# Kernel tuning notes

Hardware: AMD Instinct MI355X
Metric: run time of the kernel (lower is better)

## Reference

```python
import jax, jax.numpy as jnp
import numpy as np

UNITS = 512
BACKCAST_LEN = 512
FORECAST_LEN = 128
NB_HARMONICS = 64  # forecast_length // 2
THETAS_DIM = 2 * NB_HARMONICS
BATCH = 16384


def _seasonality_basis(length, nb_harmonics):
    # t = 2*pi*arange(L)/L ; rows interleaved [cos(0*t), sin(0*t), cos(1*t), sin(1*t), ...]
    t = 2.0 * np.pi * jnp.arange(length, dtype=jnp.float32) / length
    i = jnp.arange(nb_harmonics, dtype=jnp.float32)[:, None]  # [H,1]
    angles = i * t[None, :]                                   # [H,L]
    basis = jnp.stack([jnp.cos(angles), jnp.sin(angles)], axis=1)  # [H,2,L]
    return basis.reshape(2 * nb_harmonics, length)            # [2H,L]


def setup_inputs() -> dict:
    key = jax.random.key(0)
    ks = jax.random.split(key, 10)
    s_in = 1.0 / np.sqrt(BACKCAST_LEN)
    s_u = 1.0 / np.sqrt(UNITS)
    return {
        "x": jax.random.normal(ks[0], (BATCH, BACKCAST_LEN), jnp.float32),
        "W1": jax.random.normal(ks[1], (UNITS, BACKCAST_LEN), jnp.float32) * s_in,
        "b1": jax.random.normal(ks[2], (UNITS,), jnp.float32) * s_in,
        "W2": jax.random.normal(ks[3], (UNITS, UNITS), jnp.float32) * s_u,
        "b2": jax.random.normal(ks[4], (UNITS,), jnp.float32) * s_u,
        "W3": jax.random.normal(ks[5], (UNITS, UNITS), jnp.float32) * s_u,
        "b3": jax.random.normal(ks[6], (UNITS,), jnp.float32) * s_u,
        "W4": jax.random.normal(ks[7], (UNITS, UNITS), jnp.float32) * s_u,
        "b4": jax.random.normal(ks[8], (UNITS,), jnp.float32) * s_u,
        "Wt": jax.random.normal(ks[9], (THETAS_DIM, UNITS), jnp.float32) * s_u,
    }


def reference(x, W1, b1, W2, b2, W3, b3, W4, b4, Wt):
    h = jax.nn.relu(x @ W1.T + b1)
    h = jax.nn.relu(h @ W2.T + b2)
    h = jax.nn.relu(h @ W3.T + b3)
    h = jax.nn.relu(h @ W4.T + b4)
    theta = h @ Wt.T  # [B, 2H], shared thetas (share_thetas=True)
    basis_b = _seasonality_basis(BACKCAST_LEN, NB_HARMONICS)  # [2H, Lb]
    basis_f = _seasonality_basis(FORECAST_LEN, NB_HARMONICS)  # [2H, Lf]
    backcast = theta @ basis_b  # [B, Lb]
    forecast = theta @ basis_f  # [B, Lf]
    return (backcast, forecast)
```

## Files before the change

kernel.cpp:

```cpp
#include <hip/hip_runtime.h>
#include <hip/hip_bf16.h>
#include <math.h>


#define BATCH 16384
#define ROWS  64

typedef __bf16 bf16x8 __attribute__((ext_vector_type(8)));
typedef float  f32x4  __attribute__((ext_vector_type(4)));

__device__ __forceinline__ unsigned short f2bf(float f) {
  union { float f; unsigned u; } v; v.f = f;
  unsigned r = v.u + 0x7fff + ((v.u >> 16) & 1);
  return (unsigned short)(r >> 16);
}

__global__ __launch_bounds__(256) void prep_kernel(
    const float* __restrict__ W1, const float* __restrict__ W2,
    const float* __restrict__ W3, const float* __restrict__ W4,
    const float* __restrict__ Wt,
    unsigned short* __restrict__ W1p, unsigned short* __restrict__ W2p,
    unsigned short* __restrict__ W3p, unsigned short* __restrict__ W4p,
    unsigned short* __restrict__ Wtp,
    unsigned short* __restrict__ basp) {
  const int t = blockIdx.x * 256 + threadIdx.x;
  if (t < 139264) {
    const float* src; unsigned short* dst; int u;
    if (t < 131072) {
      const int w = t >> 15; u = t & 32767;
      src = (w == 0) ? W1 : (w == 1) ? W2 : (w == 2) ? W3 : W4;
      dst = (w == 0) ? W1p : (w == 1) ? W2p : (w == 2) ? W3p : W4p;
    } else {
      u = t - 131072; src = Wt; dst = Wtp;
    }
    const int lane = u & 63, ks = (u >> 6) & 15, cf = u >> 10;
    const int col = cf * 16 + (lane & 15);
    const int k0  = ks * 32 + (lane >> 4) * 8;
    const float4* s = (const float4*)(src + (size_t)col * 512 + k0);
    const float4 a = s[0], b = s[1];
    uint4 o;
    o.x = f2bf(a.x) | ((unsigned)f2bf(a.y) << 16);
    o.y = f2bf(a.z) | ((unsigned)f2bf(a.w) << 16);
    o.z = f2bf(b.x) | ((unsigned)f2bf(b.y) << 16);
    o.w = f2bf(b.z) | ((unsigned)f2bf(b.w) << 16);
    ((uint4*)dst)[u] = o;
  } else if (t < 149504) {
    const int u = t - 139264;
    const int lane = u & 63, ks = (u >> 6) & 3, cf = u >> 8;
    const int col = cf * 16 + (lane & 15);
    const int r0  = ks * 32 + (lane >> 4) * 8;
    int l, L;
    if (col < 512) { l = col; L = 512; } else { l = col - 512; L = 128; }
    const float w0 = 6.283185307179586f * (float)l / (float)L;
    unsigned short e[8];
#pragma unroll
    for (int i = 0; i < 8; ++i) {
      const int r = r0 + i;
      const float ang = (float)(r >> 1) * w0;
      e[i] = f2bf((r & 1) ? sinf(ang) : cosf(ang));
    }
    uint4 o;
    o.x = e[0] | ((unsigned)e[1] << 16);
    o.y = e[2] | ((unsigned)e[3] << 16);
    o.z = e[4] | ((unsigned)e[5] << 16);
    o.w = e[6] | ((unsigned)e[7] << 16);
    ((uint4*)basp)[u] = o;
  }
}

__device__ __forceinline__ void layer512(
    unsigned short* hA, const bf16x8* __restrict__ Wp,
    const float* __restrict__ bias, const int wv, const int lane) {
  const int l15 = lane & 15, g = lane >> 4;
  int rb[4], am[4];
#pragma unroll
  for (int m = 0; m < 4; ++m) {
    const int row = m * 16 + l15;
    rb[m] = row * 1024;
    am[m] = (row & 7) << 4;
  }
  f32x4 acc[4][4];
#pragma unroll
  for (int m = 0; m < 4; ++m)
#pragma unroll
    for (int n = 0; n < 4; ++n) acc[m][n] = (f32x4){0.f, 0.f, 0.f, 0.f};

  const bf16x8* base = Wp + (size_t)wv * 4096 + lane;

  bf16x8 bv[4][4];
#pragma unroll
  for (int s = 0; s < 3; ++s)
#pragma unroll
    for (int n = 0; n < 4; ++n) bv[s][n] = base[n * 1024 + s * 64];

#pragma unroll
  for (int ks = 0; ks < 16; ++ks) {
    if (ks < 13) {
#pragma unroll
      for (int n = 0; n < 4; ++n)
        bv[(ks + 3) & 3][n] = base[n * 1024 + (ks + 3) * 64];
    }
    bf16x8 av[4];
    const int kb = ks * 64 + g * 16;
#pragma unroll
    for (int m = 0; m < 4; ++m)
      av[m] = *(const bf16x8*)((const char*)hA + rb[m] + (kb ^ am[m]));
    __builtin_amdgcn_s_setprio(1);
#pragma unroll
    for (int m = 0; m < 4; ++m)
#pragma unroll
      for (int n = 0; n < 4; ++n)
        acc[m][n] = __builtin_amdgcn_mfma_f32_16x16x32_bf16(av[m], bv[ks & 3][n], acc[m][n], 0, 0, 0);
    __builtin_amdgcn_s_setprio(0);
  }

  __syncthreads();
#pragma unroll
  for (int n = 0; n < 4; ++n) {
    const int col = wv * 64 + n * 16 + l15;
    const float bvv = bias[col];
#pragma unroll
    for (int m = 0; m < 4; ++m)
#pragma unroll
      for (int r = 0; r < 4; ++r) {
        const int row = m * 16 + g * 4 + r;
        const float v = fmaxf(acc[m][n][r] + bvv, 0.f);
        *(unsigned short*)((char*)hA + row * 1024 + ((col * 2) ^ ((row & 7) << 4))) = f2bf(v);
      }
  }
  __syncthreads();
}

__global__ __launch_bounds__(512, 2) void fused_nbeats(
    const float* __restrict__ x,
    const bf16x8* __restrict__ W1p, const float* __restrict__ b1,
    const bf16x8* __restrict__ W2p, const float* __restrict__ b2,
    const bf16x8* __restrict__ W3p, const float* __restrict__ b3,
    const bf16x8* __restrict__ W4p, const float* __restrict__ b4,
    const bf16x8* __restrict__ Wtp,
    const bf16x8* __restrict__ basp,
    float* __restrict__ out) {
  __shared__ __align__(16) unsigned short hA[ROWS * 512];

  const int tid  = threadIdx.x;
  const int lane = tid & 63;
  const int wv   = tid >> 6;
  const int l15  = lane & 15, g = lane >> 4;
  const int r0   = blockIdx.x * ROWS;

  {
    const float4* xs = (const float4*)(x + (size_t)r0 * 512);
#pragma unroll
    for (int j = 0; j < 16; ++j) {
      const int f = tid + j * 512;
      const int row = f >> 7, c4 = f & 127;
      const float4 v = xs[f];
      uint2 o;
      o.x = f2bf(v.x) | ((unsigned)f2bf(v.y) << 16);
      o.y = f2bf(v.z) | ((unsigned)f2bf(v.w) << 16);
      *(uint2*)((char*)hA + row * 1024 + ((c4 * 8) ^ ((row & 7) << 4))) = o;
    }
  }
  __syncthreads();

  layer512(hA, W1p, b1, wv, lane);
  layer512(hA, W2p, b2, wv, lane);
  layer512(hA, W3p, b3, wv, lane);
  layer512(hA, W4p, b4, wv, lane);

  {
    int rb[4], am[4];
#pragma unroll
    for (int m = 0; m < 4; ++m) {
      const int row = m * 16 + l15;
      rb[m] = row * 1024;
      am[m] = (row & 7) << 4;
    }
    f32x4 tacc[4];
#pragma unroll
    for (int m = 0; m < 4; ++m) tacc[m] = (f32x4){0.f, 0.f, 0.f, 0.f};
    const bf16x8* tb = Wtp + (size_t)wv * 1024 + lane;
    bf16x8 tv[4];
#pragma unroll
    for (int s = 0; s < 3; ++s) tv[s] = tb[s * 64];
#pragma unroll
    for (int ks = 0; ks < 16; ++ks) {
      if (ks < 13) tv[(ks + 3) & 3] = tb[(ks + 3) * 64];
      bf16x8 av[4];
      const int kb = ks * 64 + g * 16;
#pragma unroll
      for (int m = 0; m < 4; ++m)
        av[m] = *(const bf16x8*)((const char*)hA + rb[m] + (kb ^ am[m]));
      __builtin_amdgcn_s_setprio(1);
#pragma unroll
      for (int m = 0; m < 4; ++m)
        tacc[m] = __builtin_amdgcn_mfma_f32_16x16x32_bf16(av[m], tv[ks & 3], tacc[m], 0, 0, 0);
      __builtin_amdgcn_s_setprio(0);
    }
    __syncthreads();
#pragma unroll
    for (int m = 0; m < 4; ++m)
#pragma unroll
      for (int r = 0; r < 4; ++r) {
        const int row = m * 16 + g * 4 + r;
        const int col = wv * 16 + l15;
        *(unsigned short*)((char*)hA + row * 256 + ((col * 2) ^ ((row & 7) << 4))) =
            f2bf(tacc[m][r]);
      }
  }
  __syncthreads();

  {
    f32x4 facc[4][5];
#pragma unroll
    for (int m = 0; m < 4; ++m)
#pragma unroll
      for (int n = 0; n < 5; ++n) facc[m][n] = (f32x4){0.f, 0.f, 0.f, 0.f};
    int rb2[4], am2[4];
#pragma unroll
    for (int m = 0; m < 4; ++m) {
      const int row = m * 16 + l15;
      rb2[m] = row * 256;
      am2[m] = (row & 7) << 4;
    }
    const bf16x8* bb = basp + (size_t)wv * 1280 + lane;
#pragma unroll
    for (int ks = 0; ks < 4; ++ks) {
      bf16x8 bvv[5];
#pragma unroll
      for (int n = 0; n < 5; ++n) bvv[n] = bb[n * 256 + ks * 64];
      bf16x8 av[4];
      const int kb = ks * 64 + g * 16;
#pragma unroll
      for (int m = 0; m < 4; ++m)
        av[m] = *(const bf16x8*)((const char*)hA + rb2[m] + (kb ^ am2[m]));
      __builtin_amdgcn_s_setprio(1);
#pragma unroll
      for (int n = 0; n < 5; ++n)
#pragma unroll
        for (int m = 0; m < 4; ++m)
          facc[m][n] = __builtin_amdgcn_mfma_f32_16x16x32_bf16(av[m], bvv[n], facc[m][n], 0, 0, 0);
      __builtin_amdgcn_s_setprio(0);
    }
#pragma unroll
    for (int n = 0; n < 5; ++n) {
      const int col = wv * 80 + n * 16 + l15;
#pragma unroll
      for (int m = 0; m < 4; ++m)
#pragma unroll
        for (int r = 0; r < 4; ++r) {
          const int row = r0 + m * 16 + g * 4 + r;
          const float v = facc[m][n][r];
          if (col < 512)
            out[(size_t)row * 512 + col] = v;
          else
            out[(size_t)BATCH * 512 + (size_t)row * 128 + (col - 512)] = v;
        }
    }
  }
}

extern "C" void kernel_launch(void* const* d_in, const int* in_sizes, int n_in,
                              void* d_out, int out_size, void* d_ws, size_t ws_size,
                              hipStream_t stream) {
  const float* x  = (const float*)d_in[0];
  const float* W1 = (const float*)d_in[1];
  const float* b1 = (const float*)d_in[2];
  const float* W2 = (const float*)d_in[3];
  const float* b2 = (const float*)d_in[4];
  const float* W3 = (const float*)d_in[5];
  const float* b3 = (const float*)d_in[6];
  const float* W4 = (const float*)d_in[7];
  const float* b4 = (const float*)d_in[8];
  const float* Wt = (const float*)d_in[9];

  unsigned short* ws  = (unsigned short*)d_ws;
  unsigned short* W1p = ws;
  unsigned short* W2p = ws + 262144;
  unsigned short* W3p = ws + 524288;
  unsigned short* W4p = ws + 786432;
  unsigned short* Wtp = ws + 1048576;
  unsigned short* basp = ws + 1114112;

  prep_kernel<<<584, 256, 0, stream>>>(W1, W2, W3, W4, Wt,
                                       W1p, W2p, W3p, W4p, Wtp, basp);
  fused_nbeats<<<BATCH / ROWS, 512, 0, stream>>>(
      x, (const bf16x8*)W1p, b1, (const bf16x8*)W2p, b2,
      (const bf16x8*)W3p, b3, (const bf16x8*)W4p, b4,
      (const bf16x8*)Wtp, (const bf16x8*)basp, (float*)d_out);
}
```

Baseline: 140.1 us.

## Ping-pong LDS activations, prefetch next-layer weights, transpose MFMA for vector stores

Activations now alternate between two LDS buffers, which removes one of the two barriers per layer. A 6-deep register ring of weight fragments carries prefetches of the next layer's first k-slices across layer boundaries. The MFMA operands are swapped so each lane owns 4 consecutive columns, letting bias loads, LDS writes and the global output stores use vector (uint2/float4) accesses. Theta and basis weights are also fully preloaded into registers. Costs are double the LDS footprint (128KB per block, which may hurt 2-block occupancy) and higher register pressure.

```diff
diff --git a/kernel.cpp b/kernel.cpp
--- a/kernel.cpp
+++ b/kernel.cpp
@@ -68,10 +68,31 @@
   }
 }
 
+__device__ __forceinline__ void wait_lds_and_barrier() {
+  asm volatile("s_waitcnt lgkmcnt(0)" ::: "memory");
+  __builtin_amdgcn_sched_barrier(0);
+  __builtin_amdgcn_s_barrier();
+  __builtin_amdgcn_sched_barrier(0);
+}
+
+template <int PHASE, bool PF_NEXT>
 __device__ __forceinline__ void layer512(
-    unsigned short* hA, const bf16x8* __restrict__ Wp,
-    const float* __restrict__ bias, const int wv, const int lane) {
+    const unsigned short* hin, unsigned short* hout,
+    const bf16x8* __restrict__ wcur, const bf16x8* __restrict__ wnext,
+    const float* __restrict__ bias, bf16x8 (&bv)[6][4],
+    const int wv, const int lane) {
   const int l15 = lane & 15, g = lane >> 4;
+  f32x4 acc[4][4];
+#pragma unroll
+  for (int m = 0; m < 4; ++m)
+#pragma unroll
+    for (int n = 0; n < 4; ++n) acc[m][n] = (f32x4){0.f, 0.f, 0.f, 0.f};
+
+  float4 bias4[4];
+#pragma unroll
+  for (int n = 0; n < 4; ++n)
+    bias4[n] = *(const float4*)(bias + wv * 64 + n * 16 + g * 4);
+
   int rb[4], am[4];
 #pragma unroll
   for (int m = 0; m < 4; ++m) {
@@ -79,56 +100,51 @@
     rb[m] = row * 1024;
     am[m] = (row & 7) << 4;
   }
-  f32x4 acc[4][4];
-#pragma unroll
-  for (int m = 0; m < 4; ++m)
-#pragma unroll
-    for (int n = 0; n < 4; ++n) acc[m][n] = (f32x4){0.f, 0.f, 0.f, 0.f};
-
-  const bf16x8* base = Wp + (size_t)wv * 4096 + lane;
-
-  bf16x8 bv[4][4];
-#pragma unroll
-  for (int s = 0; s < 3; ++s)
-#pragma unroll
-    for (int n = 0; n < 4; ++n) bv[s][n] = base[n * 1024 + s * 64];
 
 #pragma unroll
   for (int ks = 0; ks < 16; ++ks) {
-    if (ks < 13) {
+    if (ks < 11) {
 #pragma unroll
       for (int n = 0; n < 4; ++n)
-        bv[(ks + 3) & 3][n] = base[n * 1024 + (ks + 3) * 64];
+        bv[(PHASE + ks + 5) % 6][n] = wcur[n * 1024 + (ks + 5) * 64];
+    } else if (PF_NEXT) {
+#pragma unroll
+      for (int n = 0; n < 4; ++n)
+        bv[(PHASE + ks + 5) % 6][n] = wnext[n * 1024 + (ks - 11) * 64];
     }
     bf16x8 av[4];
     const int kb = ks * 64 + g * 16;
 #pragma unroll
     for (int m = 0; m < 4; ++m)
-      av[m] = *(const bf16x8*)((const char*)hA + rb[m] + (kb ^ am[m]));
+      av[m] = *(const bf16x8*)((const char*)hin + rb[m] + (kb ^ am[m]));
     __builtin_amdgcn_s_setprio(1);
 #pragma unroll
     for (int m = 0; m < 4; ++m)
 #pragma unroll
       for (int n = 0; n < 4; ++n)
-        acc[m][n] = __builtin_amdgcn_mfma_f32_16x16x32_bf16(av[m], bv[ks & 3][n], acc[m][n], 0, 0, 0);
+        acc[m][n] = __builtin_amdgcn_mfma_f32_16x16x32_bf16(
+            bv[(PHASE + ks) % 6][n], av[m], acc[m][n], 0, 0, 0);
     __builtin_amdgcn_s_setprio(0);
   }
 
-  __syncthreads();
-#pragma unroll
-  for (int n = 0; n < 4; ++n) {
-    const int col = wv * 64 + n * 16 + l15;
-    const float bvv = bias[col];
-#pragma unroll
-    for (int m = 0; m < 4; ++m)
-#pragma unroll
-      for (int r = 0; r < 4; ++r) {
-        const int row = m * 16 + g * 4 + r;
-        const float v = fmaxf(acc[m][n][r] + bvv, 0.f);
-        *(unsigned short*)((char*)hA + row * 1024 + ((col * 2) ^ ((row & 7) << 4))) = f2bf(v);
-      }
-  }
-  __syncthreads();
+#pragma unroll
+  for (int m = 0; m < 4; ++m) {
+    const int row = m * 16 + l15;
+    const int sw  = (row & 7) << 4;
+#pragma unroll
+    for (int n = 0; n < 4; ++n) {
+      const float v0 = fmaxf(acc[m][n][0] + bias4[n].x, 0.f);
+      const float v1 = fmaxf(acc[m][n][1] + bias4[n].y, 0.f);
+      const float v2 = fmaxf(acc[m][n][2] + bias4[n].z, 0.f);
+      const float v3 = fmaxf(acc[m][n][3] + bias4[n].w, 0.f);
+      uint2 o;
+      o.x = f2bf(v0) | ((unsigned)f2bf(v1) << 16);
+      o.y = f2bf(v2) | ((unsigned)f2bf(v3) << 16);
+      const int c0 = (wv * 64 + n * 16 + g * 4) * 2;
+      *(uint2*)((char*)hout + row * 1024 + (c0 ^ sw)) = o;
+    }
+  }
+  wait_lds_and_barrier();
 }
 
 __global__ __launch_bounds__(512, 2) void fused_nbeats(
@@ -140,13 +156,25 @@
     const bf16x8* __restrict__ Wtp,
     const bf16x8* __restrict__ basp,
     float* __restrict__ out) {
-  __shared__ __align__(16) unsigned short hA[ROWS * 512];
+  __shared__ __align__(16) unsigned short h0[ROWS * 512];
+  __shared__ __align__(16) unsigned short h1[ROWS * 512];
 
   const int tid  = threadIdx.x;
   const int lane = tid & 63;
   const int wv   = tid >> 6;
   const int l15  = lane & 15, g = lane >> 4;
   const int r0   = blockIdx.x * ROWS;
+
+  const bf16x8* w1 = W1p + (size_t)wv * 4096 + lane;
+  const bf16x8* w2 = W2p + (size_t)wv * 4096 + lane;
+  const bf16x8* w3 = W3p + (size_t)wv * 4096 + lane;
+  const bf16x8* w4 = W4p + (size_t)wv * 4096 + lane;
+
+  bf16x8 bv[6][4];
+#pragma unroll
+  for (int s = 0; s < 5; ++s)
+#pragma unroll
+    for (int n = 0; n < 4; ++n) bv[s][n] = w1[n * 1024 + s * 64];
 
   {
     const float4* xs = (const float4*)(x + (size_t)r0 * 512);
@@ -158,17 +186,22 @@
       uint2 o;
       o.x = f2bf(v.x) | ((unsigned)f2bf(v.y) << 16);
       o.y = f2bf(v.z) | ((unsigned)f2bf(v.w) << 16);
-      *(uint2*)((char*)hA + row * 1024 + ((c4 * 8) ^ ((row & 7) << 4))) = o;
-    }
-  }
-  __syncthreads();
-
-  layer512(hA, W1p, b1, wv, lane);
-  layer512(hA, W2p, b2, wv, lane);
-  layer512(hA, W3p, b3, wv, lane);
-  layer512(hA, W4p, b4, wv, lane);
+      *(uint2*)((char*)h0 + row * 1024 + ((c4 * 8) ^ ((row & 7) << 4))) = o;
+    }
+  }
+  wait_lds_and_barrier();
+
+  layer512<0, true >(h0, h1, w1, w2, b1, bv, wv, lane);
+  layer512<4, true >(h1, h0, w2, w3, b2, bv, wv, lane);
+  layer512<2, true >(h0, h1, w3, w4, b3, bv, wv, lane);
+  layer512<0, false>(h1, h0, w4, (const bf16x8*)0, b4, bv, wv, lane);
 
   {
+    const bf16x8* tb = Wtp + (size_t)wv * 1024 + lane;
+    bf16x8 tv[16];
+#pragma unroll
+    for (int s = 0; s < 16; ++s) tv[s] = tb[s * 64];
+
     int rb[4], am[4];
 #pragma unroll
     for (int m = 0; m < 4; ++m) {
@@ -179,38 +212,41 @@
     f32x4 tacc[4];
 #pragma unroll
     for (int m = 0; m < 4; ++m) tacc[m] = (f32x4){0.f, 0.f, 0.f, 0.f};
-    const bf16x8* tb = Wtp + (size_t)wv * 1024 + lane;
-    bf16x8 tv[4];
-#pragma unroll
-    for (int s = 0; s < 3; ++s) tv[s] = tb[s * 64];
 #pragma unroll
     for (int ks = 0; ks < 16; ++ks) {
-      if (ks < 13) tv[(ks + 3) & 3] = tb[(ks + 3) * 64];
       bf16x8 av[4];
       const int kb = ks * 64 + g * 16;
 #pragma unroll
       for (int m = 0; m < 4; ++m)
-        av[m] = *(const bf16x8*)((const char*)hA + rb[m] + (kb ^ am[m]));
+        av[m] = *(const bf16x8*)((const char*)h0 + rb[m] + (kb ^ am[m]));
       __builtin_amdgcn_s_setprio(1);
 #pragma unroll
       for (int m = 0; m < 4; ++m)
-        tacc[m] = __builtin_amdgcn_mfma_f32_16x16x32_bf16(av[m], tv[ks & 3], tacc[m], 0, 0, 0);
+        tacc[m] = __builtin_amdgcn_mfma_f32_16x16x32_bf16(
+            tv[ks], av[m], tacc[m], 0, 0, 0);
       __builtin_amdgcn_s_setprio(0);
     }
-    __syncthreads();
-#pragma unroll
-    for (int m = 0; m < 4; ++m)
-#pragma unroll
-      for (int r = 0; r < 4; ++r) {
-        const int row = m * 16 + g * 4 + r;
-        const int col = wv * 16 + l15;
-        *(unsigned short*)((char*)hA + row * 256 + ((col * 2) ^ ((row & 7) << 4))) =
-            f2bf(tacc[m][r]);
-      }
-  }
-  __syncthreads();
+#pragma unroll
+    for (int m = 0; m < 4; ++m) {
+      const int row = m * 16 + l15;
+      const int sw  = (row & 7) << 4;
+      uint2 o;
+      o.x = f2bf(tacc[m][0]) | ((unsigned)f2bf(tacc[m][1]) << 16);
+      o.y = f2bf(tacc[m][2]) | ((unsigned)f2bf(tacc[m][3]) << 16);
+      const int c0 = (wv * 16 + g * 4) * 2;
+      *(uint2*)((char*)h1 + row * 256 + (c0 ^ sw)) = o;
+    }
+  }
+  wait_lds_and_barrier();
 
   {
+    const bf16x8* bb = basp + (size_t)wv * 1280 + lane;
+    bf16x8 bvv[5][4];
+#pragma unroll
+    for (int n = 0; n < 5; ++n)
+#pragma unroll
+      for (int ks = 0; ks < 4; ++ks) bvv[n][ks] = bb[n * 256 + ks * 64];
+
     f32x4 facc[4][5];
 #pragma unroll
     for (int m = 0; m < 4; ++m)
@@ -223,39 +259,35 @@
       rb2[m] = row * 256;
       am2[m] = (row & 7) << 4;
     }
-    const bf16x8* bb = basp + (size_t)wv * 1280 + lane;
 #pragma unroll
     for (int ks = 0; ks < 4; ++ks) {
-      bf16x8 bvv[5];
-#pragma unroll
-      for (int n = 0; n < 5; ++n) bvv[n] = bb[n * 256 + ks * 64];
       bf16x8 av[4];
       const int kb = ks * 64 + g * 16;
 #pragma unroll
       for (int m = 0; m < 4; ++m)
-        av[m] = *(const bf16x8*)((const char*)hA + rb2[m] + (kb ^ am2[m]));
+        av[m] = *(const bf16x8*)((const char*)h1 + rb2[m] + (kb ^ am2[m]));
       __builtin_amdgcn_s_setprio(1);
 #pragma unroll
       for (int n = 0; n < 5; ++n)
 #pragma unroll
         for (int m = 0; m < 4; ++m)
-          facc[m][n] = __builtin_amdgcn_mfma_f32_16x16x32_bf16(av[m], bvv[n], facc[m][n], 0, 0, 0);
+          facc[m][n] = __builtin_amdgcn_mfma_f32_16x16x32_bf16(
+              bvv[n][ks], av[m], facc[m][n], 0, 0, 0);
       __builtin_amdgcn_s_setprio(0);
     }
 #pragma unroll
     for (int n = 0; n < 5; ++n) {
-      const int col = wv * 80 + n * 16 + l15;
-#pragma unroll
-      for (int m = 0; m < 4; ++m)
-#pragma unroll
-        for (int r = 0; r < 4; ++r) {
-          const int row = r0 + m * 16 + g * 4 + r;
-          const float v = facc[m][n][r];
-          if (col < 512)
-            out[(size_t)row * 512 + col] = v;
-          else
-            out[(size_t)BATCH * 512 + (size_t)row * 128 + (col - 512)] = v;
-        }
+      const int c0 = wv * 80 + n * 16 + g * 4;
+#pragma unroll
+      for (int m = 0; m < 4; ++m) {
+        const int row = r0 + m * 16 + l15;
+        float4 o = make_float4(facc[m][n][0], facc[m][n][1],
+                               facc[m][n][2], facc[m][n][3]);
+        if (c0 < 512)
+          *(float4*)(out + (size_t)row * 512 + c0) = o;
+        else
+          *(float4*)(out + (size_t)BATCH * 512 + (size_t)row * 128 + (c0 - 512)) = o;
+      }
     }
   }
 }
```

Measured after the change: 153.2 us. 9.4% more time.
